# Kernel tuning notes

Hardware: AMD Instinct MI355X
Metric: run time of the kernel (lower is better)

Reference implementation:

```python
import jax, jax.numpy as jnp
import numpy as np

D_MODEL = 2048
N_HEADS = 16
D_HEAD = D_MODEL // N_HEADS


def setup_inputs() -> dict:
    key = jax.random.key(0)
    k1, k2, k3, k4, k5 = jax.random.split(key, 5)
    x = jax.random.normal(k1, (4, 2048, D_MODEL), dtype=jnp.float32)
    s = 1.0 / np.sqrt(D_MODEL)
    qkv_w = jax.random.normal(k2, (3 * D_MODEL, D_MODEL), dtype=jnp.float32) * s
    qkv_b = jax.random.normal(k3, (3 * D_MODEL,), dtype=jnp.float32) * 0.01
    out_w = jax.random.normal(k4, (D_MODEL, D_MODEL), dtype=jnp.float32) * s
    out_b = jax.random.normal(k5, (D_MODEL,), dtype=jnp.float32) * 0.01
    return {"x": x, "qkv_w": qkv_w, "qkv_b": qkv_b, "out_w": out_w, "out_b": out_b}


def reference(x, qkv_w, qkv_b, out_w, out_b):
    B, T, D = x.shape
    # fused QKV projection: (B,T,D) -> (B,T,3D), torch Linear uses W^T
    qkv = jnp.einsum('btd,ed->bte', x, qkv_w) + qkv_b
    qkv = qkv.reshape(B, T, 3, N_HEADS, D_HEAD)
    qkv = jnp.transpose(qkv, (2, 0, 3, 1, 4))  # (3, B, H, T, Dh)
    q, k, v = qkv[0], qkv[1], qkv[2]
    # scaled dot-product attention (non-causal)
    scale = 1.0 / jnp.sqrt(jnp.asarray(D_HEAD, dtype=x.dtype))
    scores = jnp.einsum('bhqd,bhkd->bhqk', q, k) * scale
    attn = jax.nn.softmax(scores, axis=-1)
    out = jnp.einsum('bhqk,bhkd->bhqd', attn, v)
    out = jnp.transpose(out, (0, 2, 1, 3)).reshape(B, T, D)
    return jnp.einsum('btd,ed->bte', out, out_w) + out_b
```

## Files before the change

kernel.cpp:

```cpp
#include <hip/hip_runtime.h>

typedef unsigned short u16;
typedef __attribute__((ext_vector_type(8))) __bf16 bf16x8;
typedef __attribute__((ext_vector_type(4))) float f32x4;

#define SEQ 2048
#define DMODEL 2048
#define NHEADS 16
#define DHEAD 128

typedef __attribute__((address_space(1))) void gvoid_t;
typedef __attribute__((address_space(3))) void lvoid_t;

__device__ inline void gload_lds16(const void* g, void* l) {
  __builtin_amdgcn_global_load_lds((gvoid_t*)g, (lvoid_t*)l, 16, 0, 0);
}

__device__ inline u16 f2bf(float f) {
  unsigned u = __float_as_uint(f);
  unsigned r = (u + 0x7fffu + ((u >> 16) & 1u)) >> 16;
  return (u16)r;
}

__global__ __launch_bounds__(256) void cvt_f32_bf16(const float* __restrict__ in,
                                                    u16* __restrict__ out, int n4) {
  int i = blockIdx.x * 256 + threadIdx.x;
  if (i >= n4) return;
  float4 v = reinterpret_cast<const float4*>(in)[i];
  ushort4 o;
  o.x = f2bf(v.x); o.y = f2bf(v.y); o.z = f2bf(v.z); o.w = f2bf(v.w);
  reinterpret_cast<ushort4*>(out)[i] = o;
}


#define GBAR() __builtin_amdgcn_s_barrier()
#define LGKM0() do { asm volatile("s_waitcnt lgkmcnt(0)" ::: "memory"); \
                     __builtin_amdgcn_sched_barrier(0); } while (0)

template <int MODE>
__global__ __launch_bounds__(512, 1) void gemm256(
    const u16* __restrict__ A, const u16* __restrict__ B,
    const float* __restrict__ bias, int M, int N, int K, int nby,
    u16* __restrict__ qb, u16* __restrict__ kb, u16* __restrict__ vtb,
    float* __restrict__ outf) {
  __shared__ __align__(16) u16 As[2][256 * 64];
  __shared__ __align__(16) u16 Bs[2][256 * 64];
  const int nwg = gridDim.x;
  const int cpx = nwg >> 3;
  const int bid = blockIdx.x;
  const int sw = (bid & 7) * cpx + (bid >> 3);
  const int bx = sw / nby, by = sw % nby;
  const int m0 = bx * 256, n0 = by * 256;
  const int tid = threadIdx.x, lane = tid & 63, w = tid >> 6;
  const int wm = w >> 2, wn = w & 3;
  const int fr = lane & 15, hi = lane >> 4;
  const int g4 = hi * 4;
  const u16* Abase = A + (size_t)m0 * K;
  const u16* Bbase = B + (size_t)n0 * K;

  f32x4 acc[8][4];
#pragma unroll
  for (int i = 0; i < 8; i++)
#pragma unroll
    for (int j = 0; j < 4; j++) acc[i][j] = f32x4{0.f, 0.f, 0.f, 0.f};

#define STAGE(T, P)                                                              \
  do {                                                                           \
    const int t64 = (T) * 64;                                                    \
    _Pragma("unroll") for (int j = 0; j < 4; j++) {                              \
      const int U = (j * 8 + w) * 64 + lane;                                     \
      const int r_ = U >> 3;                                                     \
      const int us = (lane & 7) ^ (r_ & 7);                                      \
      gload_lds16(Abase + (size_t)r_ * K + t64 + us * 8, &As[P][U * 8]);         \
      gload_lds16(Bbase + (size_t)r_ * K + t64 + us * 8, &Bs[P][U * 8]);         \
    }                                                                            \
  } while (0)

#define LDA(AF, H, P)                                                            \
  do {                                                                           \
    _Pragma("unroll") for (int fi = 0; fi < 4; fi++) {                           \
      const int row = wm * 128 + (H) * 64 + fi * 16 + fr;                        \
      _Pragma("unroll") for (int kk = 0; kk < 2; kk++) {                         \
        const int u = (kk * 4 + hi) ^ (row & 7);                                 \
        AF[fi][kk] = *(const bf16x8*)&As[P][row * 64 + u * 8];                    \
      }                                                                          \
    }                                                                            \
  } while (0)

#define LDB(BF, G, P)                                                            \
  do {                                                                           \
    _Pragma("unroll") for (int fj = 0; fj < 2; fj++) {                           \
      const int row = wn * 64 + (G) * 32 + fj * 16 + fr;                         \
      _Pragma("unroll") for (int kk = 0; kk < 2; kk++) {                         \
        const int u = (kk * 4 + hi) ^ (row & 7);                                 \
        BF[fj][kk] = *(const bf16x8*)&Bs[P][row * 64 + u * 8];                    \
      }                                                                          \
    }                                                                            \
  } while (0)

#define MF(AF, BF, H, G)                                                         \
  do {                                                                           \
    __builtin_amdgcn_s_setprio(1);                                               \
    _Pragma("unroll") for (int fi = 0; fi < 4; fi++)                             \
    _Pragma("unroll") for (int fj = 0; fj < 2; fj++)                             \
    _Pragma("unroll") for (int kk = 0; kk < 2; kk++)                             \
      acc[(H) * 4 + fi][(G) * 2 + fj] = __builtin_amdgcn_mfma_f32_16x16x32_bf16( \
          AF[fi][kk], BF[fj][kk], acc[(H) * 4 + fi][(G) * 2 + fj], 0, 0, 0);     \
    __builtin_amdgcn_s_setprio(0);                                               \
  } while (0)

  const int NT = K >> 6;
  STAGE(0, 0);
  STAGE(1, 1);
  asm volatile("s_waitcnt vmcnt(8)" ::: "memory");
  __builtin_amdgcn_sched_barrier(0);
  GBAR();

  bf16x8 a[4][2], b0[2][2], b1[2][2];
  for (int t = 0; t < NT; t++) {
    const int p = t & 1;
    LDA(a, 0, p);
    LDB(b0, 0, p);
    GBAR(); LGKM0();
    MF(a, b0, 0, 0);
    GBAR();
    LDB(b1, 1, p);
    GBAR(); LGKM0();
    MF(a, b1, 0, 1);
    GBAR();
    LDA(a, 1, p);
    GBAR(); LGKM0();
    MF(a, b0, 1, 0);
    GBAR();
    if (t + 2 < NT) STAGE(t + 2, p);
    GBAR();
    MF(a, b1, 1, 1);
    if (t + 2 < NT) {
      asm volatile("s_waitcnt vmcnt(8)" ::: "memory");
    } else if (t + 1 < NT) {
      asm volatile("s_waitcnt vmcnt(0)" ::: "memory");
    }
    __builtin_amdgcn_sched_barrier(0);
    GBAR();
  }

  if (MODE == 0) {
    const int which = n0 >> 11;
#pragma unroll
    for (int mi = 0; mi < 8; mi++) {
      const int trow = m0 + wm * 128 + mi * 16 + g4;
      const int b = trow >> 11;
      const int t = trow & 2047;
#pragma unroll
      for (int nj = 0; nj < 4; nj++) {
        const int col = n0 + wn * 64 + nj * 16 + fr;
        const int h = (col >> 7) & 15;
        const int dh = col & 127;
        const float bv = bias[col];
        if (which == 2) {
          ushort4 pk;
          pk.x = f2bf(acc[mi][nj][0] + bv);
          pk.y = f2bf(acc[mi][nj][1] + bv);
          pk.z = f2bf(acc[mi][nj][2] + bv);
          pk.w = f2bf(acc[mi][nj][3] + bv);
          *reinterpret_cast<ushort4*>(vtb + ((size_t)(b * NHEADS + h) * DHEAD + dh) * SEQ + t) = pk;
        } else {
          u16* dst = (which == 0) ? qb : kb;
          const float sc = (which == 0) ? 0.08838834764831845f : 1.0f;
#pragma unroll
          for (int r = 0; r < 4; r++)
            dst[((size_t)(b * NHEADS + h) * SEQ + (t + r)) * DHEAD + dh] =
                f2bf((acc[mi][nj][r] + bv) * sc);
        }
      }
    }
  } else {
#pragma unroll
    for (int mi = 0; mi < 8; mi++) {
      const int row = m0 + wm * 128 + mi * 16 + g4;
#pragma unroll
      for (int nj = 0; nj < 4; nj++) {
        const int col = n0 + wn * 64 + nj * 16 + fr;
        const float bv = bias[col];
#pragma unroll
        for (int r = 0; r < 4; r++) outf[(size_t)(row + r) * N + col] = acc[mi][nj][r] + bv;
      }
    }
  }
#undef STAGE
#undef LDA
#undef LDB
#undef MF
}

__global__ __launch_bounds__(256, 2) void attn_fwd(const u16* __restrict__ Q,
                                                   const u16* __restrict__ Kb,
                                                   const u16* __restrict__ VT,
                                                   u16* __restrict__ O) {
  __shared__ __align__(16) u16 Ks[64 * 128];
  __shared__ __align__(16) u16 Vs[128 * 64];
  __shared__ __align__(16) u16 P_lds[4][32][72];
  const int bh = blockIdx.y;
  const int b = bh >> 4, h = bh & 15;
  const int w = threadIdx.x >> 6;
  const int lane = threadIdx.x & 63;
  const int fr = lane & 15;
  const int hi = lane >> 4;
  const int kr = hi * 8;
  const int g4 = hi * 4;
  const int q0w = blockIdx.x * 128 + w * 32;

  const u16* Qp = Q + (size_t)bh * SEQ * DHEAD;
  const u16* Kp = Kb + (size_t)bh * SEQ * DHEAD;
  const u16* Vp = VT + (size_t)bh * DHEAD * SEQ;

  bf16x8 qf[2][4];
#pragma unroll
  for (int mg = 0; mg < 2; mg++)
#pragma unroll
    for (int kk = 0; kk < 4; kk++)
      qf[mg][kk] = *(const bf16x8*)(Qp + (size_t)(q0w + mg * 16 + fr) * DHEAD + kk * 32 + kr);

  f32x4 oacc[2][8];
#pragma unroll
  for (int mg = 0; mg < 2; mg++)
#pragma unroll
    for (int i = 0; i < 8; i++) oacc[mg][i] = f32x4{0.f, 0.f, 0.f, 0.f};
  float mrun[2][4] = {{-1e30f, -1e30f, -1e30f, -1e30f}, {-1e30f, -1e30f, -1e30f, -1e30f}};
  float lrun[2][4] = {{0.f, 0.f, 0.f, 0.f}, {0.f, 0.f, 0.f, 0.f}};

  bf16x8 kreg[4], vreg[4];
#pragma unroll
  for (int i = 0; i < 4; i++) {
    const int u = w * 256 + i * 64 + lane;
    const int rK = u >> 4, c16 = u & 15;
    kreg[i] = *(const bf16x8*)(Kp + (size_t)rK * DHEAD + c16 * 8);
    const int rV = u >> 3, c8 = u & 7;
    vreg[i] = *(const bf16x8*)(Vp + (size_t)rV * SEQ + c8 * 8);
  }

  for (int kv0 = 0; kv0 < SEQ; kv0 += 64) {
    __syncthreads();
#pragma unroll
    for (int i = 0; i < 4; i++) {
      const int u = w * 256 + i * 64 + lane;
      const int rK = u >> 4, c16 = u & 15;
      *(bf16x8*)&Ks[rK * 128 + ((c16 ^ (rK & 7)) * 8)] = kreg[i];
      const int rV = u >> 3, c8 = u & 7;
      *(bf16x8*)&Vs[rV * 64 + ((c8 ^ (rV & 7)) * 8)] = vreg[i];
    }
    __syncthreads();
    if (kv0 + 64 < SEQ) {
      const int kvn = kv0 + 64;
#pragma unroll
      for (int i = 0; i < 4; i++) {
        const int u = w * 256 + i * 64 + lane;
        const int rK = u >> 4, c16 = u & 15;
        kreg[i] = *(const bf16x8*)(Kp + (size_t)(kvn + rK) * DHEAD + c16 * 8);
        const int rV = u >> 3, c8 = u & 7;
        vreg[i] = *(const bf16x8*)(Vp + (size_t)rV * SEQ + kvn + c8 * 8);
      }
    }

    f32x4 s[2][4];
#pragma unroll
    for (int mg = 0; mg < 2; mg++)
#pragma unroll
      for (int ct = 0; ct < 4; ct++) s[mg][ct] = f32x4{0.f, 0.f, 0.f, 0.f};
    __builtin_amdgcn_s_setprio(1);
#pragma unroll
    for (int ct = 0; ct < 4; ct++) {
      const int row = ct * 16 + fr;
#pragma unroll
      for (int kk = 0; kk < 4; kk++) {
        bf16x8 kf = *(const bf16x8*)&Ks[row * 128 + (((kk * 4 + hi) ^ (row & 7)) * 8)];
        s[0][ct] = __builtin_amdgcn_mfma_f32_16x16x32_bf16(qf[0][kk], kf, s[0][ct], 0, 0, 0);
        s[1][ct] = __builtin_amdgcn_mfma_f32_16x16x32_bf16(qf[1][kk], kf, s[1][ct], 0, 0, 0);
      }
    }
    __builtin_amdgcn_s_setprio(0);

    float sf[2][4];
#pragma unroll
    for (int mg = 0; mg < 2; mg++) {
#pragma unroll
      for (int r = 0; r < 4; r++) {
        float mx = fmaxf(fmaxf(s[mg][0][r], s[mg][1][r]), fmaxf(s[mg][2][r], s[mg][3][r]));
#pragma unroll
        for (int d = 1; d < 16; d <<= 1) mx = fmaxf(mx, __shfl_xor(mx, d, 64));
        float nm = fmaxf(mrun[mg][r], mx);
        sf[mg][r] = __expf(mrun[mg][r] - nm);
        mrun[mg][r] = nm;
      }
#pragma unroll
      for (int ct = 0; ct < 4; ct++)
#pragma unroll
        for (int r = 0; r < 4; r++) s[mg][ct][r] = __expf(s[mg][ct][r] - mrun[mg][r]);
#pragma unroll
      for (int r = 0; r < 4; r++) {
        float su = s[mg][0][r] + s[mg][1][r] + s[mg][2][r] + s[mg][3][r];
#pragma unroll
        for (int d = 1; d < 16; d <<= 1) su += __shfl_xor(su, d, 64);
        lrun[mg][r] = lrun[mg][r] * sf[mg][r] + su;
      }
#pragma unroll
      for (int dt = 0; dt < 8; dt++) {
        oacc[mg][dt][0] *= sf[mg][0]; oacc[mg][dt][1] *= sf[mg][1];
        oacc[mg][dt][2] *= sf[mg][2]; oacc[mg][dt][3] *= sf[mg][3];
      }
#pragma unroll
      for (int ct = 0; ct < 4; ct++)
#pragma unroll
        for (int r = 0; r < 4; r++)
          P_lds[w][mg * 16 + g4 + r][ct * 16 + fr] = f2bf(s[mg][ct][r]);
    }

    bf16x8 pf[2][2];
#pragma unroll
    for (int mg = 0; mg < 2; mg++)
#pragma unroll
      for (int kk = 0; kk < 2; kk++)
        pf[mg][kk] = *(const bf16x8*)&P_lds[w][mg * 16 + fr][kk * 32 + kr];
    __builtin_amdgcn_s_setprio(1);
#pragma unroll
    for (int dt = 0; dt < 8; dt++) {
      const int row = dt * 16 + fr;
#pragma unroll
      for (int kk = 0; kk < 2; kk++) {
        bf16x8 vf = *(const bf16x8*)&Vs[row * 64 + (((kk * 4 + hi) ^ (row & 7)) * 8)];
        oacc[0][dt] = __builtin_amdgcn_mfma_f32_16x16x32_bf16(pf[0][kk], vf, oacc[0][dt], 0, 0, 0);
        oacc[1][dt] = __builtin_amdgcn_mfma_f32_16x16x32_bf16(pf[1][kk], vf, oacc[1][dt], 0, 0, 0);
      }
    }
    __builtin_amdgcn_s_setprio(0);
  }

#pragma unroll
  for (int mg = 0; mg < 2; mg++)
#pragma unroll
    for (int r = 0; r < 4; r++) {
      float inv = 1.0f / lrun[mg][r];
      const int t = q0w + mg * 16 + g4 + r;
      u16* op = O + ((size_t)(b * SEQ + t)) * DMODEL + h * DHEAD;
#pragma unroll
      for (int dt = 0; dt < 8; dt++) op[dt * 16 + fr] = f2bf(oacc[mg][dt][r] * inv);
    }
}

extern "C" void kernel_launch(void* const* d_in, const int* in_sizes, int n_in,
                              void* d_out, int out_size, void* d_ws, size_t ws_size,
                              hipStream_t stream) {
  const float* x = (const float*)d_in[0];
  const float* qkv_w = (const float*)d_in[1];
  const float* qkv_b = (const float*)d_in[2];
  const float* out_w = (const float*)d_in[3];
  const float* out_b = (const float*)d_in[4];
  float* out = (float*)d_out;

  char* ws = (char*)d_ws;
  u16* xb = (u16*)ws;
  u16* wqkv = (u16*)(ws + 33554432);
  u16* qb = (u16*)(ws + 33554432 + 25165824);
  u16* kb = qb + (size_t)64 * SEQ * DHEAD;
  u16* vtb = kb + (size_t)64 * SEQ * DHEAD;
  u16* attnb = xb;
  u16* outwb = wqkv;

  cvt_f32_bf16<<<16777216 / 4 / 256, 256, 0, stream>>>(x, xb, 16777216 / 4);
  cvt_f32_bf16<<<12582912 / 4 / 256, 256, 0, stream>>>(qkv_w, wqkv, 12582912 / 4);
  gemm256<0><<<768, 512, 0, stream>>>(xb, wqkv, qkv_b, 8192, 6144, 2048, 24, qb, kb, vtb,
                                      nullptr);
  cvt_f32_bf16<<<4194304 / 4 / 256, 256, 0, stream>>>(out_w, outwb, 4194304 / 4);
  dim3 ga(SEQ / 128, 64);
  attn_fwd<<<ga, 256, 0, stream>>>(qb, kb, vtb, attnb);
  gemm256<1><<<256, 512, 0, stream>>>(attnb, outwb, out_b, 8192, 2048, 2048, 8, nullptr,
                                      nullptr, nullptr, out);
}
```

Before: 570.5 us.

## Transpose QK^T MFMA and skip online-softmax rescale unless max grows past threshold

Swaps the MFMA operands so each lane holds a query row's scores across four keys. Row max and sum now need only two cross-lane shuffles instead of four per row, and P can be written to LDS as packed 4-element stores. It also adds a lazy rescale: the running max and the accumulator rescale are updated only when some row's new max exceeds the stored max by more than 8. This removes exp and multiply work on most iterations, at the cost of some numerical headroom in exp and a wave-level branch.

Measured after the change: 500.3 us. 12.3% less time.

```diff
diff --git a/kernel.cpp b/kernel.cpp
--- a/kernel.cpp
+++ b/kernel.cpp
@@ -31,7 +31,6 @@
   o.x = f2bf(v.x); o.y = f2bf(v.y); o.z = f2bf(v.z); o.w = f2bf(v.w);
   reinterpret_cast<ushort4*>(out)[i] = o;
 }
-
 
 #define GBAR() __builtin_amdgcn_s_barrier()
 #define LGKM0() do { asm volatile("s_waitcnt lgkmcnt(0)" ::: "memory"); \
@@ -226,8 +225,8 @@
   for (int mg = 0; mg < 2; mg++)
 #pragma unroll
     for (int i = 0; i < 8; i++) oacc[mg][i] = f32x4{0.f, 0.f, 0.f, 0.f};
-  float mrun[2][4] = {{-1e30f, -1e30f, -1e30f, -1e30f}, {-1e30f, -1e30f, -1e30f, -1e30f}};
-  float lrun[2][4] = {{0.f, 0.f, 0.f, 0.f}, {0.f, 0.f, 0.f, 0.f}};
+  float mrun[2] = {-1e30f, -1e30f};
+  float lrun[2] = {0.f, 0.f};
 
   bf16x8 kreg[4], vreg[4];
 #pragma unroll
@@ -274,45 +273,65 @@
 #pragma unroll
       for (int kk = 0; kk < 4; kk++) {
         bf16x8 kf = *(const bf16x8*)&Ks[row * 128 + (((kk * 4 + hi) ^ (row & 7)) * 8)];
-        s[0][ct] = __builtin_amdgcn_mfma_f32_16x16x32_bf16(qf[0][kk], kf, s[0][ct], 0, 0, 0);
-        s[1][ct] = __builtin_amdgcn_mfma_f32_16x16x32_bf16(qf[1][kk], kf, s[1][ct], 0, 0, 0);
+        s[0][ct] = __builtin_amdgcn_mfma_f32_16x16x32_bf16(kf, qf[0][kk], s[0][ct], 0, 0, 0);
+        s[1][ct] = __builtin_amdgcn_mfma_f32_16x16x32_bf16(kf, qf[1][kk], s[1][ct], 0, 0, 0);
       }
     }
     __builtin_amdgcn_s_setprio(0);
 
-    float sf[2][4];
+    float pm[2];
 #pragma unroll
     for (int mg = 0; mg < 2; mg++) {
-#pragma unroll
-      for (int r = 0; r < 4; r++) {
-        float mx = fmaxf(fmaxf(s[mg][0][r], s[mg][1][r]), fmaxf(s[mg][2][r], s[mg][3][r]));
-#pragma unroll
-        for (int d = 1; d < 16; d <<= 1) mx = fmaxf(mx, __shfl_xor(mx, d, 64));
-        float nm = fmaxf(mrun[mg][r], mx);
-        sf[mg][r] = __expf(mrun[mg][r] - nm);
-        mrun[mg][r] = nm;
-      }
+      f32x4 mv = s[mg][0];
+      mv[0] = fmaxf(mv[0], s[mg][1][0]); mv[1] = fmaxf(mv[1], s[mg][1][1]);
+      mv[2] = fmaxf(mv[2], s[mg][1][2]); mv[3] = fmaxf(mv[3], s[mg][1][3]);
+      mv[0] = fmaxf(mv[0], s[mg][2][0]); mv[1] = fmaxf(mv[1], s[mg][2][1]);
+      mv[2] = fmaxf(mv[2], s[mg][2][2]); mv[3] = fmaxf(mv[3], s[mg][2][3]);
+      mv[0] = fmaxf(mv[0], s[mg][3][0]); mv[1] = fmaxf(mv[1], s[mg][3][1]);
+      mv[2] = fmaxf(mv[2], s[mg][3][2]); mv[3] = fmaxf(mv[3], s[mg][3][3]);
+      float p = fmaxf(fmaxf(mv[0], mv[1]), fmaxf(mv[2], mv[3]));
+      p = fmaxf(p, __shfl_xor(p, 16, 64));
+      p = fmaxf(p, __shfl_xor(p, 32, 64));
+      pm[mg] = p;
+    }
+
+    const bool need = (pm[0] - mrun[0] > 8.f) || (pm[1] - mrun[1] > 8.f);
+    if (__any(need)) {
+#pragma unroll
+      for (int mg = 0; mg < 2; mg++) {
+        float nm = fmaxf(mrun[mg], pm[mg]);
+        float sfv = __expf(mrun[mg] - nm);
+        mrun[mg] = nm;
+        lrun[mg] *= sfv;
+        float fac[4];
+#pragma unroll
+        for (int r = 0; r < 4; r++) fac[r] = __shfl(sfv, g4 + r, 64);
+#pragma unroll
+        for (int dt = 0; dt < 8; dt++) {
+          oacc[mg][dt][0] *= fac[0]; oacc[mg][dt][1] *= fac[1];
+          oacc[mg][dt][2] *= fac[2]; oacc[mg][dt][3] *= fac[3];
+        }
+      }
+    }
+
+#pragma unroll
+    for (int mg = 0; mg < 2; mg++) {
 #pragma unroll
       for (int ct = 0; ct < 4; ct++)
 #pragma unroll
-        for (int r = 0; r < 4; r++) s[mg][ct][r] = __expf(s[mg][ct][r] - mrun[mg][r]);
-#pragma unroll
-      for (int r = 0; r < 4; r++) {
-        float su = s[mg][0][r] + s[mg][1][r] + s[mg][2][r] + s[mg][3][r];
-#pragma unroll
-        for (int d = 1; d < 16; d <<= 1) su += __shfl_xor(su, d, 64);
-        lrun[mg][r] = lrun[mg][r] * sf[mg][r] + su;
-      }
-#pragma unroll
-      for (int dt = 0; dt < 8; dt++) {
-        oacc[mg][dt][0] *= sf[mg][0]; oacc[mg][dt][1] *= sf[mg][1];
-        oacc[mg][dt][2] *= sf[mg][2]; oacc[mg][dt][3] *= sf[mg][3];
-      }
-#pragma unroll
-      for (int ct = 0; ct < 4; ct++)
-#pragma unroll
-        for (int r = 0; r < 4; r++)
-          P_lds[w][mg * 16 + g4 + r][ct * 16 + fr] = f2bf(s[mg][ct][r]);
+        for (int r = 0; r < 4; r++) s[mg][ct][r] = __expf(s[mg][ct][r] - mrun[mg]);
+      f32x4 sv = s[mg][0] + s[mg][1] + s[mg][2] + s[mg][3];
+      float su = (sv[0] + sv[1]) + (sv[2] + sv[3]);
+      su += __shfl_xor(su, 16, 64);
+      su += __shfl_xor(su, 32, 64);
+      lrun[mg] += su;
+#pragma unroll
+      for (int ct = 0; ct < 4; ct++) {
+        ushort4 pk;
+        pk.x = f2bf(s[mg][ct][0]); pk.y = f2bf(s[mg][ct][1]);
+        pk.z = f2bf(s[mg][ct][2]); pk.w = f2bf(s[mg][ct][3]);
+        *reinterpret_cast<ushort4*>(&P_lds[w][mg * 16 + fr][ct * 16 + g4]) = pk;
+      }
     }
 
     bf16x8 pf[2][2];
@@ -336,15 +355,19 @@
   }
 
 #pragma unroll
-  for (int mg = 0; mg < 2; mg++)
+  for (int mg = 0; mg < 2; mg++) {
+    float linv = 1.0f / lrun[mg];
+    float fac[4];
+#pragma unroll
+    for (int r = 0; r < 4; r++) fac[r] = __shfl(linv, g4 + r, 64);
 #pragma unroll
     for (int r = 0; r < 4; r++) {
-      float inv = 1.0f / lrun[mg][r];
       const int t = q0w + mg * 16 + g4 + r;
       u16* op = O + ((size_t)(b * SEQ + t)) * DMODEL + h * DHEAD;
 #pragma unroll
-      for (int dt = 0; dt < 8; dt++) op[dt * 16 + fr] = f2bf(oacc[mg][dt][r] * inv);
-    }
+      for (int dt = 0; dt < 8; dt++) op[dt * 16 + fr] = f2bf(oacc[mg][dt][r] * fac[r]);
+    }
+  }
 }
 
 extern "C" void kernel_launch(void* const* d_in, const int* in_sizes, int n_in,
```
